# Performance work log

Measured on AMD Instinct MI355X. Metric: run time of the kernel, lower is better.

## Reference

```python
import jax, jax.numpy as jnp
import numpy as np
from jax.scipy.special import logsumexp

SINKHORN_ALPHA = 20.0
OT_MAX_ITER = 100
STOP_THR = 0.005


def setup_inputs() -> dict:
    key = jax.random.key(0)
    k1, k2 = jax.random.split(key)
    x = jax.random.normal(k1, (256, 384), dtype=jnp.float32)   # topic embeddings [K, D]
    y = jax.random.normal(k2, (32768, 384), dtype=jnp.float32)  # word embeddings  [V, D]
    return {"x": x, "y": y}


def reference(x, y):
    n, m = x.shape[0], y.shape[0]
    # FASTopic pairwise_euclidean_distance: squared euclidean cost [n, m]
    M = jnp.sum(x * x, axis=1, keepdims=True) + jnp.sum(y * y, axis=1) - 2.0 * (x @ y.T)
    a = jnp.full((n, 1), 1.0 / n, dtype=M.dtype)
    b = jnp.full((m, 1), 1.0 / m, dtype=M.dtype)
    log_a = jnp.log(a + 1e-30)
    log_b = jnp.log(b + 1e-30)
    log_K0 = -M * SINKHORN_ALPHA

    # State trick: the original mutates log_K only at the periodic absorption step
    # (log_K += log_u + log_v.T). We keep log_K = log_K0 + cum_u + cum_v.T so the
    # carried state is only O(n + m) vectors; math is identical.
    def body(state):
        log_u, log_v, cum_u, cum_v, err, cpt = state
        log_K = log_K0 + cum_u + cum_v.T                                    # [n, m]
        log_v_n = log_b - logsumexp(log_K.T + log_u.T, axis=1)[:, None]     # [m, 1]
        log_u_n = log_a - logsumexp(log_K + log_v_n.T, axis=1)[:, None]     # [n, 1]
        cpt_n = cpt + 1

        def absorb(_):
            cu = cum_u + log_u_n
            cv = cum_v + log_v_n
            lK = log_K0 + cu + cv.T
            # marginal check with log_u = log_v = 0 (matches check_convergence)
            row = jnp.exp(logsumexp(lK, axis=1))[:, None]
            col = jnp.exp(logsumexp(lK, axis=0))[:, None]
            e = jnp.maximum(jnp.max(jnp.abs(row - a)), jnp.max(jnp.abs(col - b)))
            return jnp.zeros_like(log_u_n), jnp.zeros_like(log_v_n), cu, cv, e

        def keep(_):
            return log_u_n, log_v_n, cum_u, cum_v, err

        lu, lv, cu, cv, e = jax.lax.cond(cpt_n % 50 == 1, absorb, keep, None)
        return (lu, lv, cu, cv, e, cpt_n)

    def cond_fn(state):
        err, cpt = state[4], state[5]
        return (err > STOP_THR) & (cpt < OT_MAX_ITER)

    init = (jnp.zeros((n, 1), M.dtype), jnp.zeros((m, 1), M.dtype),
            jnp.zeros((n, 1), M.dtype), jnp.zeros((m, 1), M.dtype),
            jnp.array(1.0, M.dtype), jnp.array(0, jnp.int32))
    log_u, log_v, cum_u, cum_v, _, _ = jax.lax.while_loop(cond_fn, body, init)

    log_K = log_K0 + cum_u + cum_v.T
    transp = jnp.exp(log_u) * (jnp.exp(log_K) * jnp.exp(log_v).T)  # diag(u) K diag(v)
    loss_ETP = jnp.sum(transp * M)
    return loss_ETP, transp
```

## Files before the change

### kernel.cpp

```cpp
#include <hip/hip_runtime.h>
#include <math.h>


#define N_TOPIC 256
#define N_WORD  32768

static constexpr float LOG_A = -5.545177444479562f;
static constexpr float LOG_B = -10.397207708399179f;
static constexpr float BVAL  = 3.0517578125e-05f;

typedef float f32x4 __attribute__((ext_vector_type(4)));
typedef short bf16x8 __attribute__((ext_vector_type(8)));

#define PIN4(v) asm volatile("" : "+v"((v).x), "+v"((v).y), "+v"((v).z), "+v"((v).w))

__global__ __launch_bounds__(256) void init_k(
    const float* __restrict__ x, const float* __restrict__ y,
    float* __restrict__ nx, float* __restrict__ ny, float* __restrict__ su,
    unsigned* __restrict__ colerr, int* __restrict__ active,
    int* __restrict__ counters, float* __restrict__ out)
{
    const int b = blockIdx.x, t = threadIdx.x;
    const int w = t >> 6, l = t & 63;
    if (b < 8192) {
        const int r = (b << 2) + w;
        const float4* y4 = (const float4*)y;
        float4 v = y4[r * 96 + l];
        float s = v.x * v.x + v.y * v.y + v.z * v.z + v.w * v.w;
        if (l < 32) {
            float4 u = y4[r * 96 + 64 + l];
            s += u.x * u.x + u.y * u.y + u.z * u.z + u.w * u.w;
        }
        for (int off = 32; off; off >>= 1) s += __shfl_down(s, off);
        if (l == 0) ny[r] = s;
    } else if (b < 8256) {
        const int r = ((b - 8192) << 2) + w;
        const float4* x4 = (const float4*)x;
        float4 v = x4[r * 96 + l];
        float s = v.x * v.x + v.y * v.y + v.z * v.z + v.w * v.w;
        if (l < 32) {
            float4 u = x4[r * 96 + 64 + l];
            s += u.x * u.x + u.y * u.y + u.z * u.z + u.w * u.w;
        }
        for (int off = 32; off; off >>= 1) s += __shfl_down(s, off);
        if (l == 0) { nx[r] = s; su[r] = -20.f * s; }
    } else {
        for (int k = t; k < 4096; k += 256) counters[k] = 0;
        if (t == 0) { colerr[0] = 0u; colerr[1] = 0u; active[0] = 1; out[0] = 0.f; }
    }
}

static __device__ __forceinline__ void split3(float v, ushort& h0, ushort& h1, ushort& h2)
{
    unsigned u0 = __float_as_uint(v);
    h0 = (ushort)(u0 >> 16);
    float r1 = v - __uint_as_float(u0 & 0xFFFF0000u);
    unsigned u1 = __float_as_uint(r1);
    h1 = (ushort)(u1 >> 16);
    float r2 = r1 - __uint_as_float(u1 & 0xFFFF0000u);
    h2 = (ushort)(__float_as_uint(r2) >> 16);
}

static __device__ __forceinline__ bool bar_arrive(int* cnt, int ph, int t, int* lastf)
{
    __threadfence();
    if (t == 0) *lastf = (atomicAdd(&cnt[ph], 1) == 255);
    __syncthreads();
    return *lastf != 0;
}
static __device__ __forceinline__ void bar_release(int* gen, int ph, int t)
{
    __threadfence();
    if (t == 0) atomicExch(gen, ph);
}
static __device__ __forceinline__ void bar_wait(int* gen, int ph, int t)
{
    if (t == 0) {
        while (atomicCAS(gen, -1, -1) < ph) __builtin_amdgcn_s_sleep(2);
    }
    __syncthreads();
    __threadfence();
}

__global__ __launch_bounds__(256, 1) void fused_k(
    const float* __restrict__ x, const float* __restrict__ y,
    float* __restrict__ su, const float* __restrict__ nx,
    const float* __restrict__ ny, float2* __restrict__ pms,
    float* __restrict__ prow, int* __restrict__ cnt, int* __restrict__ gen,
    unsigned* __restrict__ colerr, int* __restrict__ active,
    float* __restrict__ out)
{
    __shared__ __align__(16) char smem[63488];
    __shared__ int lastf;
    float4* xs4 = (float4*)smem;
    ushort* ys0 = (ushort*)(smem + 32768);
    ushort* ys1 = (ushort*)(smem + 43008);
    ushort* ys2 = (ushort*)(smem + 53248);
    float* su_lds = (float*)smem;
    float* mm    = (float*)(smem + 1024);
    float* ss    = (float*)(smem + 5120);
    float* Mcol  = (float*)(smem + 9216);
    float* Wlds  = (float*)(smem + 9728);
    float* ecol  = (float*)(smem + 10240);
    float* Rlds  = (float*)(smem + 10752);
    float* errb  = (float*)(smem + 11776);
    float* nxl   = (float*)(smem + 12288);
    float* nyl   = (float*)(smem + 13312);
    float* pq    = (float*)(smem + 13824);
    float* cv    = pq;

    const int t  = threadIdx.x;
    const int b  = blockIdx.x;
    const int w  = t >> 6, ln = t & 63, q = ln >> 4, l15 = ln & 15;
    const int jq = t & 31, ig = t >> 5, c0 = jq << 2;
    const int jy0 = b << 7;
    int ph = 1;

    const float4* x4 = (const float4*)x;
    const float4* y4 = (const float4*)y;

    f32x4 acc[4][8];
#pragma unroll
    for (int mi = 0; mi < 4; ++mi)
#pragma unroll
        for (int nj = 0; nj < 8; ++nj) acc[mi][nj] = (f32x4){0.f, 0.f, 0.f, 0.f};

    for (int kc = 0; kc < 12; ++kc) {
        __syncthreads();
#pragma unroll
        for (int p = 0; p < 8; ++p) {
            const int f = (p << 8) + t;
            const int r = f >> 3, c4 = f & 7;
            xs4[(r << 3) + (c4 ^ (r & 7))] = x4[r * 96 + (kc << 3) + c4];
        }
#pragma unroll
        for (int p = 0; p < 4; ++p) {
            const int f = (p << 8) + t;
            const int r = f >> 3, c4 = f & 7;
            float4 vy = y4[(size_t)(jy0 + r) * 96 + (kc << 3) + c4];
            ushort a0,a1,a2,b0,b1,b2,g0,g1,g2,d0,d1,d2;
            split3(vy.x, a0,a1,a2); split3(vy.y, b0,b1,b2);
            split3(vy.z, g0,g1,g2); split3(vy.w, d0,d1,d2);
            *(ushort4*)&ys0[r * 40 + (c4 << 2)] = make_ushort4(a0,b0,g0,d0);
            *(ushort4*)&ys1[r * 40 + (c4 << 2)] = make_ushort4(a1,b1,g1,d1);
            *(ushort4*)&ys2[r * 40 + (c4 << 2)] = make_ushort4(a2,b2,g2,d2);
        }
        __syncthreads();

        union U8 { ushort u[8]; bf16x8 v; };
        bf16x8 A0[4], A1[4], A2[4];
#pragma unroll
        for (int mi = 0; mi < 4; ++mi) {
            const int row = (w << 6) + (mi << 4) + l15;
            const int base = row << 3;
            float4 xa = xs4[base + (((q << 1) + 0) ^ (row & 7))];
            float4 xb = xs4[base + (((q << 1) + 1) ^ (row & 7))];
            U8 u0, u1, u2;
            split3(xa.x, u0.u[0], u1.u[0], u2.u[0]);
            split3(xa.y, u0.u[1], u1.u[1], u2.u[1]);
            split3(xa.z, u0.u[2], u1.u[2], u2.u[2]);
            split3(xa.w, u0.u[3], u1.u[3], u2.u[3]);
            split3(xb.x, u0.u[4], u1.u[4], u2.u[4]);
            split3(xb.y, u0.u[5], u1.u[5], u2.u[5]);
            split3(xb.z, u0.u[6], u1.u[6], u2.u[6]);
            split3(xb.w, u0.u[7], u1.u[7], u2.u[7]);
            A0[mi] = u0.v; A1[mi] = u1.v; A2[mi] = u2.v;
        }
#pragma unroll
        for (int nj = 0; nj < 8; ++nj) {
            const int off = ((nj << 4) + l15) * 40 + (q << 3);
            bf16x8 B0 = *(const bf16x8*)&ys0[off];
            bf16x8 B1 = *(const bf16x8*)&ys1[off];
            bf16x8 B2 = *(const bf16x8*)&ys2[off];
#pragma unroll
            for (int mi = 0; mi < 4; ++mi) {
                f32x4 c = acc[mi][nj];
                c = __builtin_amdgcn_mfma_f32_16x16x32_bf16(A0[mi], B0, c, 0, 0, 0);
                c = __builtin_amdgcn_mfma_f32_16x16x32_bf16(A0[mi], B1, c, 0, 0, 0);
                c = __builtin_amdgcn_mfma_f32_16x16x32_bf16(A1[mi], B0, c, 0, 0, 0);
                c = __builtin_amdgcn_mfma_f32_16x16x32_bf16(A1[mi], B1, c, 0, 0, 0);
                c = __builtin_amdgcn_mfma_f32_16x16x32_bf16(A0[mi], B2, c, 0, 0, 0);
                c = __builtin_amdgcn_mfma_f32_16x16x32_bf16(A2[mi], B0, c, 0, 0, 0);
                acc[mi][nj] = c;
            }
        }
    }

    float4 tile[32];
#pragma unroll
    for (int c = 0; c < 4; ++c) {
        __syncthreads();
        if (w == c) {
#pragma unroll
            for (int mi = 0; mi < 4; ++mi) {
                const int rl = (mi << 4) + (q << 2);
#pragma unroll
                for (int nj = 0; nj < 8; ++nj) {
                    const int col = (nj << 4) + l15;
#pragma unroll
                    for (int r = 0; r < 4; ++r)
                        cv[(rl + r) * 132 + col] = 40.f * acc[mi][nj][r];
                }
            }
        }
        __syncthreads();
#pragma unroll
        for (int kk = 0; kk < 8; ++kk) {
            const int il = ig + (kk << 3);
            tile[(c << 3) + kk] = *(const float4*)&cv[il * 132 + c0];
        }
    }
#pragma unroll
    for (int k = 0; k < 32; ++k) PIN4(tile[k]);

    __syncthreads();
    su_lds[t] = su[t];
    __syncthreads();

    {
        float m0=-INFINITY,m1=-INFINITY,m2=-INFINITY,m3=-INFINITY;
#pragma unroll
        for (int k = 0; k < 32; ++k) {
            const float sk = su_lds[ig + (k << 3)];
            m0=fmaxf(m0,tile[k].x+sk); m1=fmaxf(m1,tile[k].y+sk);
            m2=fmaxf(m2,tile[k].z+sk); m3=fmaxf(m3,tile[k].w+sk);
        }
        float s0=0.f,s1=0.f,s2=0.f,s3=0.f;
#pragma unroll
        for (int k = 0; k < 32; ++k) {
            const float sk = su_lds[ig + (k << 3)];
            s0+=__expf(tile[k].x+sk-m0); s1+=__expf(tile[k].y+sk-m1);
            s2+=__expf(tile[k].z+sk-m2); s3+=__expf(tile[k].w+sk-m3);
        }
        mm[ig*128+c0+0]=m0; ss[ig*128+c0+0]=s0;
        mm[ig*128+c0+1]=m1; ss[ig*128+c0+1]=s1;
        mm[ig*128+c0+2]=m2; ss[ig*128+c0+2]=s2;
        mm[ig*128+c0+3]=m3; ss[ig*128+c0+3]=s3;
        __syncthreads();
        if (t < 128) {
            float m=-INFINITY, s=0.f;
#pragma unroll
            for (int qq = 0; qq < 8; ++qq) {
                float pmv=mm[qq*128+t], psv=ss[qq*128+t];
                float nm=fmaxf(m,pmv);
                s = s*__expf(m-nm) + psv*__expf(pmv-nm);
                m = nm;
            }
            Wlds[t] = LOG_B - (m + __logf(s));
        }
        __syncthreads();
    }
    {
#pragma unroll
        for (int k = 0; k < 32; ++k) {
            const int i = ig + (k << 3);
            float a0=tile[k].x+Wlds[c0], a1=tile[k].y+Wlds[c0+1];
            float a2=tile[k].z+Wlds[c0+2], a3=tile[k].w+Wlds[c0+3];
            pq[i*33+jq] = fmaxf(fmaxf(a0,a1), fmaxf(a2,a3));
        }
        __syncthreads();
        {
            float R=-INFINITY;
#pragma unroll
            for (int qq = 0; qq < 32; ++qq) R = fmaxf(R, pq[t*33+qq]);
            Rlds[t] = R;
        }
        __syncthreads();
#pragma unroll
        for (int k = 0; k < 32; ++k) {
            const int i = ig + (k << 3);
            const float Rr = Rlds[i];
            float s = __expf(tile[k].x+Wlds[c0]-Rr)   + __expf(tile[k].y+Wlds[c0+1]-Rr)
                    + __expf(tile[k].z+Wlds[c0+2]-Rr) + __expf(tile[k].w+Wlds[c0+3]-Rr);
            pq[i*33+jq] = s;
        }
        __syncthreads();
        {
            float s = 0.f;
#pragma unroll
            for (int qq = 0; qq < 32; ++qq) s += pq[t*33+qq];
            pms[(b << 8) + t] = make_float2(Rlds[t], s);
        }
    }
    if (bar_arrive(cnt, ph, t, &lastf)) {
        __threadfence();
        float m=-INFINITY, s=0.f;
        for (int p = 0; p < 256; ++p) {
            float2 v = pms[(p << 8) + t];
            float nm = fmaxf(m, v.x);
            s = s*__expf(m-nm) + v.y*__expf(v.x-nm);
            m = nm;
        }
        su[t] = LOG_A - (m + __logf(s));
        bar_release(gen, ph, t);
    }
    bar_wait(gen, ph, t); ++ph;
    su_lds[t] = su[t];
    __syncthreads();

    int act;
    {
        float m0=-INFINITY,m1=-INFINITY,m2=-INFINITY,m3=-INFINITY;
#pragma unroll
        for (int k = 0; k < 32; ++k) {
            const float sk = su_lds[ig + (k << 3)];
            m0=fmaxf(m0,tile[k].x+sk); m1=fmaxf(m1,tile[k].y+sk);
            m2=fmaxf(m2,tile[k].z+sk); m3=fmaxf(m3,tile[k].w+sk);
        }
        float s0=0.f,s1=0.f,s2=0.f,s3=0.f;
#pragma unroll
        for (int k = 0; k < 32; ++k) {
            const float sk = su_lds[ig + (k << 3)];
            s0+=__expf(tile[k].x+sk-m0); s1+=__expf(tile[k].y+sk-m1);
            s2+=__expf(tile[k].z+sk-m2); s3+=__expf(tile[k].w+sk-m3);
        }
        mm[ig*128+c0+0]=m0; ss[ig*128+c0+0]=s0;
        mm[ig*128+c0+1]=m1; ss[ig*128+c0+1]=s1;
        mm[ig*128+c0+2]=m2; ss[ig*128+c0+2]=s2;
        mm[ig*128+c0+3]=m3; ss[ig*128+c0+3]=s3;
        __syncthreads();
        if (t < 128) {
            float m=-INFINITY, s=0.f;
#pragma unroll
            for (int qq = 0; qq < 8; ++qq) {
                float pmv=mm[qq*128+t], psv=ss[qq*128+t];
                float nm=fmaxf(m,pmv);
                s = s*__expf(m-nm) + psv*__expf(pmv-nm);
                m = nm;
            }
            errb[t] = fabsf(__expf((m + __logf(s)) + Wlds[t]) - BVAL);
        }
        __syncthreads();
        for (int n = 64; n; n >>= 1) {
            if (t < n) errb[t] = fmaxf(errb[t], errb[t + n]);
            __syncthreads();
        }
        if (t == 0) atomicMax(&colerr[0], __float_as_uint(errb[0]));
        if (bar_arrive(cnt, ph, t, &lastf)) {
            if (t == 0) {
                unsigned e = atomicMax(&colerr[0], 0u);
                active[0] = (__uint_as_float(e) > 0.005f) ? 1 : 0;
            }
            bar_release(gen, ph, t);
        }
        bar_wait(gen, ph, t); ++ph;
        act = active[0];
    }

    if (act) {
#pragma unroll 1
        for (int tt = 2; tt <= 100; ++tt) {
            {
                float m0=-INFINITY,m1=-INFINITY,m2=-INFINITY,m3=-INFINITY;
#pragma unroll
                for (int k = 0; k < 32; ++k) {
                    const float sk = su_lds[ig + (k << 3)];
                    m0=fmaxf(m0,tile[k].x+sk); m1=fmaxf(m1,tile[k].y+sk);
                    m2=fmaxf(m2,tile[k].z+sk); m3=fmaxf(m3,tile[k].w+sk);
                }
                mm[ig*128+c0+0]=m0; mm[ig*128+c0+1]=m1;
                mm[ig*128+c0+2]=m2; mm[ig*128+c0+3]=m3;
                __syncthreads();
                if (t < 128) {
                    float m=-INFINITY;
#pragma unroll
                    for (int qq = 0; qq < 8; ++qq) m = fmaxf(m, mm[qq*128+t]);
                    Mcol[t] = m;
                }
                __syncthreads();
            }
            float4 E[32];
            {
                const float Mc0=Mcol[c0], Mc1=Mcol[c0+1], Mc2=Mcol[c0+2], Mc3=Mcol[c0+3];
                float s0=0.f,s1=0.f,s2=0.f,s3=0.f;
#pragma unroll
                for (int k = 0; k < 32; ++k) {
                    const float sk = su_lds[ig + (k << 3)];
                    E[k].x=__expf(tile[k].x+sk-Mc0); s0+=E[k].x;
                    E[k].y=__expf(tile[k].y+sk-Mc1); s1+=E[k].y;
                    E[k].z=__expf(tile[k].z+sk-Mc2); s2+=E[k].z;
                    E[k].w=__expf(tile[k].w+sk-Mc3); s3+=E[k].w;
                }
                ss[ig*128+c0+0]=s0; ss[ig*128+c0+1]=s1;
                ss[ig*128+c0+2]=s2; ss[ig*128+c0+3]=s3;
                __syncthreads();
                if (t < 128) {
                    float ssum = 0.f;
#pragma unroll
                    for (int qq = 0; qq < 8; ++qq) ssum += ss[qq*128+t];
                    Wlds[t] = LOG_B - (Mcol[t] + __logf(ssum));
                    ecol[t] = 1.0f / ssum;
                }
                __syncthreads();
            }
            {
                const float e0=ecol[c0], e1=ecol[c0+1], e2=ecol[c0+2], e3=ecol[c0+3];
#pragma unroll
                for (int k = 0; k < 32; ++k) {
                    const int i = ig + (k << 3);
                    pq[i*33+jq] = E[k].x*e0 + E[k].y*e1 + E[k].z*e2 + E[k].w*e3;
                }
                __syncthreads();
                float s = 0.f;
#pragma unroll
                for (int qq = 0; qq < 32; ++qq) s += pq[t*33+qq];
                prow[(b << 8) + t] = s;
            }
            if (bar_arrive(cnt, ph, t, &lastf)) {
                __threadfence();
                float tot = 0.f;
                for (int p = 0; p < 256; ++p) tot += prow[(p << 8) + t];
                su[t] = (LOG_A - LOG_B) + su_lds[t] - __logf(tot);
                bar_release(gen, ph, t);
            }
            bar_wait(gen, ph, t); ++ph;
            su_lds[t] = su[t];
            __syncthreads();

            if (tt == 51) {
                float m0=-INFINITY,m1=-INFINITY,m2=-INFINITY,m3=-INFINITY;
#pragma unroll
                for (int k = 0; k < 32; ++k) {
                    const float sk = su_lds[ig + (k << 3)];
                    m0=fmaxf(m0,tile[k].x+sk); m1=fmaxf(m1,tile[k].y+sk);
                    m2=fmaxf(m2,tile[k].z+sk); m3=fmaxf(m3,tile[k].w+sk);
                }
                float s0=0.f,s1=0.f,s2=0.f,s3=0.f;
#pragma unroll
                for (int k = 0; k < 32; ++k) {
                    const float sk = su_lds[ig + (k << 3)];
                    s0+=__expf(tile[k].x+sk-m0); s1+=__expf(tile[k].y+sk-m1);
                    s2+=__expf(tile[k].z+sk-m2); s3+=__expf(tile[k].w+sk-m3);
                }
                mm[ig*128+c0+0]=m0; ss[ig*128+c0+0]=s0;
                mm[ig*128+c0+1]=m1; ss[ig*128+c0+1]=s1;
                mm[ig*128+c0+2]=m2; ss[ig*128+c0+2]=s2;
                mm[ig*128+c0+3]=m3; ss[ig*128+c0+3]=s3;
                __syncthreads();
                if (t < 128) {
                    float m=-INFINITY, s=0.f;
#pragma unroll
                    for (int qq = 0; qq < 8; ++qq) {
                        float pmv=mm[qq*128+t], psv=ss[qq*128+t];
                        float nm=fmaxf(m,pmv);
                        s = s*__expf(m-nm) + psv*__expf(pmv-nm);
                        m = nm;
                    }
                    errb[t] = fabsf(__expf((m + __logf(s)) + Wlds[t]) - BVAL);
                }
                __syncthreads();
                for (int n = 64; n; n >>= 1) {
                    if (t < n) errb[t] = fmaxf(errb[t], errb[t + n]);
                    __syncthreads();
                }
                if (t == 0) atomicMax(&colerr[1], __float_as_uint(errb[0]));
                if (bar_arrive(cnt, ph, t, &lastf)) {
                    if (t == 0) {
                        unsigned e = atomicMax(&colerr[1], 0u);
                        active[0] = (__uint_as_float(e) > 0.005f) ? 1 : 0;
                    }
                    bar_release(gen, ph, t);
                }
                bar_wait(gen, ph, t); ++ph;
                if (active[0] == 0) break;
            }
        }
    }

    nxl[t] = nx[t];
    if (t < 128) nyl[t] = ny[jy0 + t];
    __syncthreads();

    float accl = 0.f;
#pragma unroll 4
    for (int k = 0; k < 32; ++k) {
        const int i = ig + (k << 3);
        const float si = su_lds[i], nxi = nxl[i];
        const float g0 = tile[k].x, g1 = tile[k].y, g2 = tile[k].z, g3 = tile[k].w;
        float v0 = __expf(g0 + si + Wlds[c0+0]);
        float v1 = __expf(g1 + si + Wlds[c0+1]);
        float v2 = __expf(g2 + si + Wlds[c0+2]);
        float v3 = __expf(g3 + si + Wlds[c0+3]);
        float* o = out + 1 + (size_t)i * 32768 + jy0 + c0;
        __builtin_nontemporal_store(v0, o + 0);
        __builtin_nontemporal_store(v1, o + 1);
        __builtin_nontemporal_store(v2, o + 2);
        __builtin_nontemporal_store(v3, o + 3);
        accl += v0 * (nxi + nyl[c0+0] - 0.05f * g0) +
                v1 * (nxi + nyl[c0+1] - 0.05f * g1) +
                v2 * (nxi + nyl[c0+2] - 0.05f * g2) +
                v3 * (nxi + nyl[c0+3] - 0.05f * g3);
    }
    for (int off = 32; off; off >>= 1) accl += __shfl_down(accl, off);
    if (ln == 0) errb[w] = accl;
    __syncthreads();
    if (t == 0) atomicAdd(out, errb[0] + errb[1] + errb[2] + errb[3]);
}

extern "C" void kernel_launch(void* const* d_in, const int* in_sizes, int n_in,
                              void* d_out, int out_size, void* d_ws, size_t ws_size,
                              hipStream_t stream)
{
    const float* x = (const float*)d_in[0];
    const float* y = (const float*)d_in[1];
    float* out = (float*)d_out;

    float* ws   = (float*)d_ws;
    float* su   = ws;
    float* nx   = su + 256;
    float* ny   = nx + 256;
    float2* pms = (float2*)(ny + 32768);
    float* prow = (float*)(pms + 65536);
    unsigned* colerr = (unsigned*)(prow + 65536);
    int* active   = (int*)(colerr + 2);
    int* counters = active + 1;
    int* gen      = counters + 3000;

    init_k<<<8257, 256, 0, stream>>>(x, y, nx, ny, su, colerr, active, counters, out);
    fused_k<<<256, 256, 0, stream>>>(x, y, su, nx, ny, pms, prow,
                                     counters, gen, colerr, active, out);
}
```

Before: 326.3 us.

## Keep Sinkhorn tile in MFMA accumulator layout instead of LDS transpose

```diff
diff --git a/kernel.cpp b/kernel.cpp
--- a/kernel.cpp
+++ b/kernel.cpp
@@ -12,7 +12,7 @@
 typedef float f32x4 __attribute__((ext_vector_type(4)));
 typedef short bf16x8 __attribute__((ext_vector_type(8)));
 
-#define PIN4(v) asm volatile("" : "+v"((v).x), "+v"((v).y), "+v"((v).z), "+v"((v).w))
+#define PINV(v) asm volatile("" : "+v"((v)[0]), "+v"((v)[1]), "+v"((v)[2]), "+v"((v)[3]))
 
 __global__ __launch_bounds__(256) void init_k(
     const float* __restrict__ x, const float* __restrict__ y,
@@ -98,26 +98,27 @@
     ushort* ys2 = (ushort*)(smem + 53248);
     float* su_lds = (float*)smem;
     float* mm    = (float*)(smem + 1024);
-    float* ss    = (float*)(smem + 5120);
-    float* Mcol  = (float*)(smem + 9216);
-    float* Wlds  = (float*)(smem + 9728);
-    float* ecol  = (float*)(smem + 10240);
-    float* Rlds  = (float*)(smem + 10752);
-    float* errb  = (float*)(smem + 11776);
-    float* nxl   = (float*)(smem + 12288);
-    float* nyl   = (float*)(smem + 13312);
-    float* pq    = (float*)(smem + 13824);
-    float* cv    = pq;
-
-    const int t  = threadIdx.x;
-    const int b  = blockIdx.x;
-    const int w  = t >> 6, ln = t & 63, q = ln >> 4, l15 = ln & 15;
-    const int jq = t & 31, ig = t >> 5, c0 = jq << 2;
+    float* ss    = (float*)(smem + 9472);
+    float* Mcol  = (float*)(smem + 17920);
+    float* Wlds  = (float*)(smem + 18432);
+    float* ecol  = (float*)(smem + 18944);
+    float* Rlds  = (float*)(smem + 19456);
+    float* errb  = (float*)(smem + 20480);
+    float* nxl   = (float*)(smem + 20992);
+    float* nyl   = (float*)(smem + 22016);
+    float* pq    = (float*)(smem + 22528);
+
+    const int t   = threadIdx.x;
+    const int b   = blockIdx.x;
+    const int w   = t >> 6, ln = t & 63, q = ln >> 4, l15 = ln & 15;
+    const int g16 = (w << 2) + q;
     const int jy0 = b << 7;
     int ph = 1;
 
     const float4* x4 = (const float4*)x;
     const float4* y4 = (const float4*)y;
+
+#define ROW(mi, r) ((w << 6) + ((mi) << 4) + (q << 2) + (r))
 
     f32x4 acc[4][8];
 #pragma unroll
@@ -185,65 +186,45 @@
             }
         }
     }
-
-    float4 tile[32];
-#pragma unroll
-    for (int c = 0; c < 4; ++c) {
-        __syncthreads();
-        if (w == c) {
-#pragma unroll
-            for (int mi = 0; mi < 4; ++mi) {
-                const int rl = (mi << 4) + (q << 2);
-#pragma unroll
-                for (int nj = 0; nj < 8; ++nj) {
-                    const int col = (nj << 4) + l15;
-#pragma unroll
-                    for (int r = 0; r < 4; ++r)
-                        cv[(rl + r) * 132 + col] = 40.f * acc[mi][nj][r];
-                }
-            }
-        }
-        __syncthreads();
-#pragma unroll
-        for (int kk = 0; kk < 8; ++kk) {
-            const int il = ig + (kk << 3);
-            tile[(c << 3) + kk] = *(const float4*)&cv[il * 132 + c0];
-        }
-    }
-#pragma unroll
-    for (int k = 0; k < 32; ++k) PIN4(tile[k]);
+#pragma unroll
+    for (int mi = 0; mi < 4; ++mi)
+#pragma unroll
+        for (int nj = 0; nj < 8; ++nj) {
+            acc[mi][nj] = acc[mi][nj] * 40.f;
+            PINV(acc[mi][nj]);
+        }
 
     __syncthreads();
     su_lds[t] = su[t];
     __syncthreads();
 
     {
-        float m0=-INFINITY,m1=-INFINITY,m2=-INFINITY,m3=-INFINITY;
-#pragma unroll
-        for (int k = 0; k < 32; ++k) {
-            const float sk = su_lds[ig + (k << 3)];
-            m0=fmaxf(m0,tile[k].x+sk); m1=fmaxf(m1,tile[k].y+sk);
-            m2=fmaxf(m2,tile[k].z+sk); m3=fmaxf(m3,tile[k].w+sk);
-        }
-        float s0=0.f,s1=0.f,s2=0.f,s3=0.f;
-#pragma unroll
-        for (int k = 0; k < 32; ++k) {
-            const float sk = su_lds[ig + (k << 3)];
-            s0+=__expf(tile[k].x+sk-m0); s1+=__expf(tile[k].y+sk-m1);
-            s2+=__expf(tile[k].z+sk-m2); s3+=__expf(tile[k].w+sk-m3);
-        }
-        mm[ig*128+c0+0]=m0; ss[ig*128+c0+0]=s0;
-        mm[ig*128+c0+1]=m1; ss[ig*128+c0+1]=s1;
-        mm[ig*128+c0+2]=m2; ss[ig*128+c0+2]=s2;
-        mm[ig*128+c0+3]=m3; ss[ig*128+c0+3]=s3;
+#pragma unroll
+        for (int nj = 0; nj < 8; ++nj) {
+            const int C = (nj << 4) + l15;
+            float m = -INFINITY;
+#pragma unroll
+            for (int mi = 0; mi < 4; ++mi)
+#pragma unroll
+                for (int r = 0; r < 4; ++r)
+                    m = fmaxf(m, acc[mi][nj][r] + su_lds[ROW(mi, r)]);
+            float s = 0.f;
+#pragma unroll
+            for (int mi = 0; mi < 4; ++mi)
+#pragma unroll
+                for (int r = 0; r < 4; ++r)
+                    s += __expf(acc[mi][nj][r] + su_lds[ROW(mi, r)] - m);
+            mm[g16 * 132 + C] = m;
+            ss[g16 * 132 + C] = s;
+        }
         __syncthreads();
         if (t < 128) {
-            float m=-INFINITY, s=0.f;
-#pragma unroll
-            for (int qq = 0; qq < 8; ++qq) {
-                float pmv=mm[qq*128+t], psv=ss[qq*128+t];
-                float nm=fmaxf(m,pmv);
-                s = s*__expf(m-nm) + psv*__expf(pmv-nm);
+            float m = -INFINITY, s = 0.f;
+#pragma unroll
+            for (int g = 0; g < 16; ++g) {
+                float pmv = mm[g * 132 + t], psv = ss[g * 132 + t];
+                float nm = fmaxf(m, pmv);
+                s = s * __expf(m - nm) + psv * __expf(pmv - nm);
                 m = nm;
             }
             Wlds[t] = LOG_B - (m + __logf(s));
@@ -251,44 +232,67 @@
         __syncthreads();
     }
     {
-#pragma unroll
-        for (int k = 0; k < 32; ++k) {
-            const int i = ig + (k << 3);
-            float a0=tile[k].x+Wlds[c0], a1=tile[k].y+Wlds[c0+1];
-            float a2=tile[k].z+Wlds[c0+2], a3=tile[k].w+Wlds[c0+3];
-            pq[i*33+jq] = fmaxf(fmaxf(a0,a1), fmaxf(a2,a3));
-        }
+        float rm[4][4];
+#pragma unroll
+        for (int mi = 0; mi < 4; ++mi)
+#pragma unroll
+            for (int r = 0; r < 4; ++r) rm[mi][r] = -INFINITY;
+#pragma unroll
+        for (int nj = 0; nj < 8; ++nj) {
+            const float Wc = Wlds[(nj << 4) + l15];
+#pragma unroll
+            for (int mi = 0; mi < 4; ++mi)
+#pragma unroll
+                for (int r = 0; r < 4; ++r)
+                    rm[mi][r] = fmaxf(rm[mi][r], acc[mi][nj][r] + Wc);
+        }
+#pragma unroll
+        for (int mi = 0; mi < 4; ++mi)
+#pragma unroll
+            for (int r = 0; r < 4; ++r)
+                pq[ROW(mi, r) * 17 + l15] = rm[mi][r];
         __syncthreads();
         {
-            float R=-INFINITY;
-#pragma unroll
-            for (int qq = 0; qq < 32; ++qq) R = fmaxf(R, pq[t*33+qq]);
+            float R = -INFINITY;
+#pragma unroll
+            for (int p = 0; p < 16; ++p) R = fmaxf(R, pq[t * 17 + p]);
             Rlds[t] = R;
         }
         __syncthreads();
-#pragma unroll
-        for (int k = 0; k < 32; ++k) {
-            const int i = ig + (k << 3);
-            const float Rr = Rlds[i];
-            float s = __expf(tile[k].x+Wlds[c0]-Rr)   + __expf(tile[k].y+Wlds[c0+1]-Rr)
-                    + __expf(tile[k].z+Wlds[c0+2]-Rr) + __expf(tile[k].w+Wlds[c0+3]-Rr);
-            pq[i*33+jq] = s;
-        }
+        float rs[4][4];
+#pragma unroll
+        for (int mi = 0; mi < 4; ++mi)
+#pragma unroll
+            for (int r = 0; r < 4; ++r) rs[mi][r] = 0.f;
+#pragma unroll
+        for (int nj = 0; nj < 8; ++nj) {
+            const float Wc = Wlds[(nj << 4) + l15];
+#pragma unroll
+            for (int mi = 0; mi < 4; ++mi)
+#pragma unroll
+                for (int r = 0; r < 4; ++r)
+                    rs[mi][r] += __expf(acc[mi][nj][r] + Wc - Rlds[ROW(mi, r)]);
+        }
+#pragma unroll
+        for (int mi = 0; mi < 4; ++mi)
+#pragma unroll
+            for (int r = 0; r < 4; ++r)
+                pq[ROW(mi, r) * 17 + l15] = rs[mi][r];
         __syncthreads();
         {
             float s = 0.f;
 #pragma unroll
-            for (int qq = 0; qq < 32; ++qq) s += pq[t*33+qq];
+            for (int p = 0; p < 16; ++p) s += pq[t * 17 + p];
             pms[(b << 8) + t] = make_float2(Rlds[t], s);
         }
     }
     if (bar_arrive(cnt, ph, t, &lastf)) {
         __threadfence();
-        float m=-INFINITY, s=0.f;
+        float m = -INFINITY, s = 0.f;
         for (int p = 0; p < 256; ++p) {
             float2 v = pms[(p << 8) + t];
             float nm = fmaxf(m, v.x);
-            s = s*__expf(m-nm) + v.y*__expf(v.x-nm);
+            s = s * __expf(m - nm) + v.y * __expf(v.x - nm);
             m = nm;
         }
         su[t] = LOG_A - (m + __logf(s));
@@ -300,32 +304,32 @@
 
     int act;
     {
-        float m0=-INFINITY,m1=-INFINITY,m2=-INFINITY,m3=-INFINITY;
-#pragma unroll
-        for (int k = 0; k < 32; ++k) {
-            const float sk = su_lds[ig + (k << 3)];
-            m0=fmaxf(m0,tile[k].x+sk); m1=fmaxf(m1,tile[k].y+sk);
-            m2=fmaxf(m2,tile[k].z+sk); m3=fmaxf(m3,tile[k].w+sk);
-        }
-        float s0=0.f,s1=0.f,s2=0.f,s3=0.f;
-#pragma unroll
-        for (int k = 0; k < 32; ++k) {
-            const float sk = su_lds[ig + (k << 3)];
-            s0+=__expf(tile[k].x+sk-m0); s1+=__expf(tile[k].y+sk-m1);
-            s2+=__expf(tile[k].z+sk-m2); s3+=__expf(tile[k].w+sk-m3);
-        }
-        mm[ig*128+c0+0]=m0; ss[ig*128+c0+0]=s0;
-        mm[ig*128+c0+1]=m1; ss[ig*128+c0+1]=s1;
-        mm[ig*128+c0+2]=m2; ss[ig*128+c0+2]=s2;
-        mm[ig*128+c0+3]=m3; ss[ig*128+c0+3]=s3;
+#pragma unroll
+        for (int nj = 0; nj < 8; ++nj) {
+            const int C = (nj << 4) + l15;
+            float m = -INFINITY;
+#pragma unroll
+            for (int mi = 0; mi < 4; ++mi)
+#pragma unroll
+                for (int r = 0; r < 4; ++r)
+                    m = fmaxf(m, acc[mi][nj][r] + su_lds[ROW(mi, r)]);
+            float s = 0.f;
+#pragma unroll
+            for (int mi = 0; mi < 4; ++mi)
+#pragma unroll
+                for (int r = 0; r < 4; ++r)
+                    s += __expf(acc[mi][nj][r] + su_lds[ROW(mi, r)] - m);
+            mm[g16 * 132 + C] = m;
+            ss[g16 * 132 + C] = s;
+        }
         __syncthreads();
         if (t < 128) {
-            float m=-INFINITY, s=0.f;
-#pragma unroll
-            for (int qq = 0; qq < 8; ++qq) {
-                float pmv=mm[qq*128+t], psv=ss[qq*128+t];
-                float nm=fmaxf(m,pmv);
-                s = s*__expf(m-nm) + psv*__expf(pmv-nm);
+            float m = -INFINITY, s = 0.f;
+#pragma unroll
+            for (int g = 0; g < 16; ++g) {
+                float pmv = mm[g * 132 + t], psv = ss[g * 132 + t];
+                float nm = fmaxf(m, pmv);
+                s = s * __expf(m - nm) + psv * __expf(pmv - nm);
                 m = nm;
             }
             errb[t] = fabsf(__expf((m + __logf(s)) + Wlds[t]) - BVAL);
@@ -350,60 +354,71 @@
     if (act) {
 #pragma unroll 1
         for (int tt = 2; tt <= 100; ++tt) {
+#pragma unroll
+            for (int nj = 0; nj < 8; ++nj) {
+                const int C = (nj << 4) + l15;
+                float m = -INFINITY;
+#pragma unroll
+                for (int mi = 0; mi < 4; ++mi)
+#pragma unroll
+                    for (int r = 0; r < 4; ++r)
+                        m = fmaxf(m, acc[mi][nj][r] + su_lds[ROW(mi, r)]);
+                mm[g16 * 132 + C] = m;
+            }
+            __syncthreads();
+            if (t < 128) {
+                float m = -INFINITY;
+#pragma unroll
+                for (int g = 0; g < 16; ++g) m = fmaxf(m, mm[g * 132 + t]);
+                Mcol[t] = m;
+            }
+            __syncthreads();
+#pragma unroll
+            for (int nj = 0; nj < 8; ++nj) {
+                const int C = (nj << 4) + l15;
+                const float Mc = Mcol[C];
+                float s = 0.f;
+#pragma unroll
+                for (int mi = 0; mi < 4; ++mi)
+#pragma unroll
+                    for (int r = 0; r < 4; ++r)
+                        s += __expf(acc[mi][nj][r] + su_lds[ROW(mi, r)] - Mc);
+                ss[g16 * 132 + C] = s;
+            }
+            __syncthreads();
+            if (t < 128) {
+                float ssum = 0.f;
+#pragma unroll
+                for (int g = 0; g < 16; ++g) ssum += ss[g * 132 + t];
+                Wlds[t] = LOG_B - (Mcol[t] + __logf(ssum));
+                ecol[t] = 1.0f / ssum;
+            }
+            __syncthreads();
             {
-                float m0=-INFINITY,m1=-INFINITY,m2=-INFINITY,m3=-INFINITY;
-#pragma unroll
-                for (int k = 0; k < 32; ++k) {
-                    const float sk = su_lds[ig + (k << 3)];
-                    m0=fmaxf(m0,tile[k].x+sk); m1=fmaxf(m1,tile[k].y+sk);
-                    m2=fmaxf(m2,tile[k].z+sk); m3=fmaxf(m3,tile[k].w+sk);
+                float rp[4][4];
+#pragma unroll
+                for (int mi = 0; mi < 4; ++mi)
+#pragma unroll
+                    for (int r = 0; r < 4; ++r) rp[mi][r] = 0.f;
+#pragma unroll
+                for (int nj = 0; nj < 8; ++nj) {
+                    const int C = (nj << 4) + l15;
+                    const float Mc = Mcol[C], ec = ecol[C];
+#pragma unroll
+                    for (int mi = 0; mi < 4; ++mi)
+#pragma unroll
+                        for (int r = 0; r < 4; ++r)
+                            rp[mi][r] += __expf(acc[mi][nj][r] + su_lds[ROW(mi, r)] - Mc) * ec;
                 }
-                mm[ig*128+c0+0]=m0; mm[ig*128+c0+1]=m1;
-                mm[ig*128+c0+2]=m2; mm[ig*128+c0+3]=m3;
-                __syncthreads();
-                if (t < 128) {
-                    float m=-INFINITY;
-#pragma unroll
-                    for (int qq = 0; qq < 8; ++qq) m = fmaxf(m, mm[qq*128+t]);
-                    Mcol[t] = m;
-                }
-                __syncthreads();
-            }
-            float4 E[32];
-            {
-                const float Mc0=Mcol[c0], Mc1=Mcol[c0+1], Mc2=Mcol[c0+2], Mc3=Mcol[c0+3];
-                float s0=0.f,s1=0.f,s2=0.f,s3=0.f;
-#pragma unroll
-                for (int k = 0; k < 32; ++k) {
-                    const float sk = su_lds[ig + (k << 3)];
-                    E[k].x=__expf(tile[k].x+sk-Mc0); s0+=E[k].x;
-                    E[k].y=__expf(tile[k].y+sk-Mc1); s1+=E[k].y;
-                    E[k].z=__expf(tile[k].z+sk-Mc2); s2+=E[k].z;
-                    E[k].w=__expf(tile[k].w+sk-Mc3); s3+=E[k].w;
-                }
-                ss[ig*128+c0+0]=s0; ss[ig*128+c0+1]=s1;
-                ss[ig*128+c0+2]=s2; ss[ig*128+c0+3]=s3;
-                __syncthreads();
-                if (t < 128) {
-                    float ssum = 0.f;
-#pragma unroll
-                    for (int qq = 0; qq < 8; ++qq) ssum += ss[qq*128+t];
-                    Wlds[t] = LOG_B - (Mcol[t] + __logf(ssum));
-                    ecol[t] = 1.0f / ssum;
-                }
-                __syncthreads();
-            }
-            {
-                const float e0=ecol[c0], e1=ecol[c0+1], e2=ecol[c0+2], e3=ecol[c0+3];
-#pragma unroll
-                for (int k = 0; k < 32; ++k) {
-                    const int i = ig + (k << 3);
-                    pq[i*33+jq] = E[k].x*e0 + E[k].y*e1 + E[k].z*e2 + E[k].w*e3;
-                }
+#pragma unroll
+                for (int mi = 0; mi < 4; ++mi)
+#pragma unroll
+                    for (int r = 0; r < 4; ++r)
+                        pq[ROW(mi, r) * 17 + l15] = rp[mi][r];
                 __syncthreads();
                 float s = 0.f;
 #pragma unroll
-                for (int qq = 0; qq < 32; ++qq) s += pq[t*33+qq];
+                for (int p = 0; p < 16; ++p) s += pq[t * 17 + p];
                 prow[(b << 8) + t] = s;
             }
             if (bar_arrive(cnt, ph, t, &lastf)) {
@@ -418,32 +433,32 @@
             __syncthreads();
 
             if (tt == 51) {
-                float m0=-INFINITY,m1=-INFINITY,m2=-INFINITY,m3=-INFINITY;
-#pragma unroll
-                for (int k = 0; k < 32; ++k) {
-                    const float sk = su_lds[ig + (k << 3)];
-                    m0=fmaxf(m0,tile[k].x+sk); m1=fmaxf(m1,tile[k].y+sk);
-                    m2=fmaxf(m2,tile[k].z+sk); m3=fmaxf(m3,tile[k].w+sk);
+#pragma unroll
+                for (int nj = 0; nj < 8; ++nj) {
+                    const int C = (nj << 4) + l15;
+                    float m = -INFINITY;
+#pragma unroll
+                    for (int mi = 0; mi < 4; ++mi)
+#pragma unroll
+                        for (int r = 0; r < 4; ++r)
+                            m = fmaxf(m, acc[mi][nj][r] + su_lds[ROW(mi, r)]);
+                    float s = 0.f;
+#pragma unroll
+                    for (int mi = 0; mi < 4; ++mi)
+#pragma unroll
+                        for (int r = 0; r < 4; ++r)
+                            s += __expf(acc[mi][nj][r] + su_lds[ROW(mi, r)] - m);
+                    mm[g16 * 132 + C] = m;
+                    ss[g16 * 132 + C] = s;
                 }
-                float s0=0.f,s1=0.f,s2=0.f,s3=0.f;
-#pragma unroll
-                for (int k = 0; k < 32; ++k) {
-                    const float sk = su_lds[ig + (k << 3)];
-                    s0+=__expf(tile[k].x+sk-m0); s1+=__expf(tile[k].y+sk-m1);
-                    s2+=__expf(tile[k].z+sk-m2); s3+=__expf(tile[k].w+sk-m3);
-                }
-                mm[ig*128+c0+0]=m0; ss[ig*128+c0+0]=s0;
-                mm[ig*128+c0+1]=m1; ss[ig*128+c0+1]=s1;
-                mm[ig*128+c0+2]=m2; ss[ig*128+c0+2]=s2;
-                mm[ig*128+c0+3]=m3; ss[ig*128+c0+3]=s3;
                 __syncthreads();
                 if (t < 128) {
-                    float m=-INFINITY, s=0.f;
-#pragma unroll
-                    for (int qq = 0; qq < 8; ++qq) {
-                        float pmv=mm[qq*128+t], psv=ss[qq*128+t];
-                        float nm=fmaxf(m,pmv);
-                        s = s*__expf(m-nm) + psv*__expf(pmv-nm);
+                    float m = -INFINITY, s = 0.f;
+#pragma unroll
+                    for (int g = 0; g < 16; ++g) {
+                        float pmv = mm[g * 132 + t], psv = ss[g * 132 + t];
+                        float nm = fmaxf(m, pmv);
+                        s = s * __expf(m - nm) + psv * __expf(pmv - nm);
                         m = nm;
                     }
                     errb[t] = fabsf(__expf((m + __logf(s)) + Wlds[t]) - BVAL);
@@ -472,24 +487,22 @@
     __syncthreads();
 
     float accl = 0.f;
-#pragma unroll 4
-    for (int k = 0; k < 32; ++k) {
-        const int i = ig + (k << 3);
-        const float si = su_lds[i], nxi = nxl[i];
-        const float g0 = tile[k].x, g1 = tile[k].y, g2 = tile[k].z, g3 = tile[k].w;
-        float v0 = __expf(g0 + si + Wlds[c0+0]);
-        float v1 = __expf(g1 + si + Wlds[c0+1]);
-        float v2 = __expf(g2 + si + Wlds[c0+2]);
-        float v3 = __expf(g3 + si + Wlds[c0+3]);
-        float* o = out + 1 + (size_t)i * 32768 + jy0 + c0;
-        __builtin_nontemporal_store(v0, o + 0);
-        __builtin_nontemporal_store(v1, o + 1);
-        __builtin_nontemporal_store(v2, o + 2);
-        __builtin_nontemporal_store(v3, o + 3);
-        accl += v0 * (nxi + nyl[c0+0] - 0.05f * g0) +
-                v1 * (nxi + nyl[c0+1] - 0.05f * g1) +
-                v2 * (nxi + nyl[c0+2] - 0.05f * g2) +
-                v3 * (nxi + nyl[c0+3] - 0.05f * g3);
+#pragma unroll
+    for (int mi = 0; mi < 4; ++mi) {
+#pragma unroll
+        for (int r = 0; r < 4; ++r) {
+            const int R = ROW(mi, r);
+            const float si = su_lds[R], nxi = nxl[R];
+            float* orow = out + 1 + (size_t)R * 32768 + jy0;
+#pragma unroll
+            for (int nj = 0; nj < 8; ++nj) {
+                const int C = (nj << 4) + l15;
+                const float g = acc[mi][nj][r];
+                const float v = __expf(g + si + Wlds[C]);
+                __builtin_nontemporal_store(v, orow + C);
+                accl += v * (nxi + nyl[C] - 0.05f * g);
+            }
+        }
     }
     for (int off = 32; off; off >>= 1) accl += __shfl_down(accl, off);
     if (ln == 0) errb[w] = accl;
```

Measured after the change: 332.3 us. No clear change (+1.8%).
